# Kernel optimization log

Measured on AMD Instinct MI355X. Metric: run time of the kernel, lower is better.

## Reference

```python
import jax, jax.numpy as jnp
import numpy as np

N_NODES = 50000
N_EDGES = 800000
D_IN = 128
D_OUT = 128
ALPHA = 0.2  # LeakyReLU negative slope


def setup_inputs() -> dict:
    key = jax.random.key(0)
    k1, k2, k3, k4 = jax.random.split(key, 4)
    x = jax.random.normal(k1, (N_NODES, D_IN), dtype=jnp.float32)
    W = jax.random.normal(k2, (D_IN, D_OUT), dtype=jnp.float32) * (1.414 / np.sqrt(D_IN))
    a = jax.random.normal(k3, (2 * D_OUT, 1), dtype=jnp.float32) * 0.1
    edge_index = jax.random.randint(k4, (2, N_EDGES), 0, N_NODES, dtype=jnp.int64)
    return {"x": x, "W": W, "a": a, "edge_index": edge_index}


def reference(x, W, a, edge_index):
    # h: (N, D_OUT)
    h = x @ W
    src, dst = edge_index[0], edge_index[1]
    # e_i = leakyrelu([h[src]; h[dst]] @ a) == leakyrelu((h@a1)[src] + (h@a2)[dst])
    a1 = a[:D_OUT, 0]
    a2 = a[D_OUT:, 0]
    s1 = h @ a1  # (N,)
    s2 = h @ a2  # (N,)
    e = jax.nn.leaky_relu(s1[src] + s2[dst], negative_slope=ALPHA)  # (E,)
    # Global softmax over all edges (faithful to F.softmax(edge_e, dim=0))
    attention = jax.nn.softmax(e)  # (E,)
    # output[dst] += attention * h[src]  (scatter-add)
    msgs = attention[:, None] * h[src]  # (E, D_OUT)
    output = jax.ops.segment_sum(msgs, dst, num_segments=N_NODES)
    return output
```

## Files before the change

### kernel.cpp

```cpp
#include <hip/hip_runtime.h>
#include <hip/hip_bf16.h>

#define N_NODES 50000
#define N_EDGES 800000
#define D 128
#define ALPHA 0.2f
#define NEG_INF -1e30f

#define KB_BLOCKS 3125
#define NSCAN_BLOCKS ((N_NODES + 255) / 256)
#define LDS_STRIDE 272

typedef __attribute__((ext_vector_type(8))) short short8;
typedef __attribute__((ext_vector_type(4))) float floatx4;

__device__ __forceinline__ unsigned int f2bf(float v)
{
    __hip_bfloat16 b = __float2bfloat16(v);
    return (unsigned int)*reinterpret_cast<unsigned short*>(&b);
}
__device__ __forceinline__ float bf_lo(unsigned int u)
{
    return __uint_as_float(u << 16);
}
__device__ __forceinline__ float bf_hi(unsigned int u)
{
    return __uint_as_float(u & 0xFFFF0000u);
}

__global__ __launch_bounds__(256) void k_wprep(
    const float* __restrict__ W, const float* __restrict__ a,
    float* __restrict__ w12)
{
    const int t = threadIdx.x;
    const int i = t & 127;
    const int which = t >> 7;
    const float* av = a + which * D;
    float acc = 0.f;
    #pragma unroll 8
    for (int j = 0; j < D; ++j)
        acc += W[(size_t)i * D + j] * av[j];
    w12[which * D + i] = acc;
}

__global__ __launch_bounds__(256) void k_fused(
    const float* __restrict__ x, const float* __restrict__ W,
    const float* __restrict__ w12, const int* __restrict__ ei,
    unsigned short* __restrict__ hb, float* __restrict__ s1,
    float* __restrict__ s2, int* __restrict__ deg, int* __restrict__ rank)
{
    __shared__ unsigned char lds[16 * LDS_STRIDE];
    const int t = threadIdx.x;
    const int rowbase = blockIdx.x * 16;

    const int r = t >> 4;
    const int c = t & 15;
    const float* xp = x + (size_t)(rowbase + r) * D + c * 8;
    const float4 v0 = *(const float4*)(xp);
    const float4 v1 = *(const float4*)(xp + 4);

    const int lane = t & 63;
    const int wv = t >> 6;
    const int q = lane >> 4;
    const int nIdx = lane & 15;
    const int n0 = wv * 32;
    short8 B[2][4];
    #pragma unroll
    for (int kt = 0; kt < 4; ++kt) {
        short8 be, bo;
        #pragma unroll
        for (int j = 0; j < 8; ++j) {
            const float* wp = W + (size_t)(kt * 32 + q * 8 + j) * D + n0 + 2 * nIdx;
            be[j] = (short)f2bf(wp[0]);
            bo[j] = (short)f2bf(wp[1]);
        }
        B[0][kt] = be;
        B[1][kt] = bo;
    }

    {
        const float* w1 = w12 + c * 8;
        const float* w2 = w12 + D + c * 8;
        float p1 = v0.x * w1[0] + v0.y * w1[1] + v0.z * w1[2] + v0.w * w1[3]
                 + v1.x * w1[4] + v1.y * w1[5] + v1.z * w1[6] + v1.w * w1[7];
        float p2 = v0.x * w2[0] + v0.y * w2[1] + v0.z * w2[2] + v0.w * w2[3]
                 + v1.x * w2[4] + v1.y * w2[5] + v1.z * w2[6] + v1.w * w2[7];
        #pragma unroll
        for (int mask = 8; mask >= 1; mask >>= 1) {
            p1 += __shfl_xor(p1, mask);
            p2 += __shfl_xor(p2, mask);
        }
        if (c == 0) { s1[rowbase + r] = p1; s2[rowbase + r] = p2; }

        uint4 pk;
        pk.x = f2bf(v0.x) | (f2bf(v0.y) << 16);
        pk.y = f2bf(v0.z) | (f2bf(v0.w) << 16);
        pk.z = f2bf(v1.x) | (f2bf(v1.y) << 16);
        pk.w = f2bf(v1.z) | (f2bf(v1.w) << 16);
        *(uint4*)(lds + r * LDS_STRIDE + c * 16) = pk;
    }
    __syncthreads();

    const unsigned char* ab = lds + nIdx * LDS_STRIDE + q * 16;
    const short8 A0 = *(const short8*)(ab);
    const short8 A1 = *(const short8*)(ab + 64);
    const short8 A2 = *(const short8*)(ab + 128);
    const short8 A3 = *(const short8*)(ab + 192);

    floatx4 acc0 = {0.f, 0.f, 0.f, 0.f};
    floatx4 acc1 = {0.f, 0.f, 0.f, 0.f};
    acc0 = __builtin_amdgcn_mfma_f32_16x16x32_bf16(A0, B[0][0], acc0, 0, 0, 0);
    acc1 = __builtin_amdgcn_mfma_f32_16x16x32_bf16(A0, B[1][0], acc1, 0, 0, 0);
    acc0 = __builtin_amdgcn_mfma_f32_16x16x32_bf16(A1, B[0][1], acc0, 0, 0, 0);
    acc1 = __builtin_amdgcn_mfma_f32_16x16x32_bf16(A1, B[1][1], acc1, 0, 0, 0);
    acc0 = __builtin_amdgcn_mfma_f32_16x16x32_bf16(A2, B[0][2], acc0, 0, 0, 0);
    acc1 = __builtin_amdgcn_mfma_f32_16x16x32_bf16(A2, B[1][2], acc1, 0, 0, 0);
    acc0 = __builtin_amdgcn_mfma_f32_16x16x32_bf16(A3, B[0][3], acc0, 0, 0, 0);
    acc1 = __builtin_amdgcn_mfma_f32_16x16x32_bf16(A3, B[1][3], acc1, 0, 0, 0);

    #pragma unroll
    for (int i = 0; i < 4; ++i) {
        const int row = rowbase + q * 4 + i;
        const unsigned int pk = f2bf(acc0[i]) | (f2bf(acc1[i]) << 16);
        *(unsigned int*)(hb + (size_t)row * D + n0 + 2 * nIdx) = pk;
    }

    const int e = blockIdx.x * 256 + t;
    rank[e] = atomicAdd(&deg[ei[N_EDGES + e]], 1);
}

__device__ __forceinline__ void online_combine(float& m, float& s,
                                               float om, float os)
{
    float nm = fmaxf(m, om);
    s = s * __expf(m - nm) + os * __expf(om - nm);
    m = nm;
}

__global__ __launch_bounds__(256) void k_scan_a(
    const int* __restrict__ deg, int* __restrict__ partials)
{
    const int i = blockIdx.x * 256 + threadIdx.x;
    int v = (i < N_NODES) ? deg[i] : 0;
    #pragma unroll
    for (int off = 32; off >= 1; off >>= 1) v += __shfl_down(v, off);
    __shared__ int ws[4];
    if ((threadIdx.x & 63) == 0) ws[threadIdx.x >> 6] = v;
    __syncthreads();
    if (threadIdx.x == 0)
        partials[blockIdx.x] = ws[0] + ws[1] + ws[2] + ws[3];
}

__global__ __launch_bounds__(256) void k_scan_b(
    const int* __restrict__ partials, int* __restrict__ partialOffs,
    int* __restrict__ offs)
{
    __shared__ int sc[256];
    const int t = threadIdx.x;
    int v = (t < NSCAN_BLOCKS) ? partials[t] : 0;
    sc[t] = v;
    __syncthreads();
    #pragma unroll
    for (int off = 1; off < 256; off <<= 1) {
        int u = (t >= off) ? sc[t - off] : 0;
        __syncthreads();
        sc[t] += u;
        __syncthreads();
    }
    if (t < NSCAN_BLOCKS) partialOffs[t] = sc[t] - v;
    if (t == 255) offs[N_NODES] = sc[255];
}

__global__ __launch_bounds__(256) void k_scan_c(
    const int* __restrict__ deg, const int* __restrict__ partialOffs,
    int* __restrict__ offs)
{
    __shared__ int sc[256];
    const int t = threadIdx.x;
    const int i = blockIdx.x * 256 + t;
    const int v = (i < N_NODES) ? deg[i] : 0;
    sc[t] = v;
    __syncthreads();
    #pragma unroll
    for (int off = 1; off < 256; off <<= 1) {
        int u = (t >= off) ? sc[t - off] : 0;
        __syncthreads();
        sc[t] += u;
        __syncthreads();
    }
    if (i < N_NODES)
        offs[i] = partialOffs[blockIdx.x] + sc[t] - v;
}

__global__ __launch_bounds__(256) void k_bucket(
    const int* __restrict__ ei, const float* __restrict__ s1,
    const float* __restrict__ s2, const int* __restrict__ offs,
    const int* __restrict__ rank, unsigned int* __restrict__ csr,
    float* __restrict__ bm, float* __restrict__ bs)
{
    const int e = blockIdx.x * 256 + threadIdx.x;
    const int sN = ei[e];
    const int dN = ei[N_EDGES + e];
    csr[offs[dN] + rank[e]] = (unsigned int)sN;

    float v = s1[sN] + s2[dN];
    v = v > 0.f ? v : ALPHA * v;

    float m = v, s = 1.f;
    #pragma unroll
    for (int off = 32; off >= 1; off >>= 1) {
        float om = __shfl_down(m, off);
        float os = __shfl_down(s, off);
        online_combine(m, s, om, os);
    }
    __shared__ float rm[4], rs[4];
    const int wid = threadIdx.x >> 6;
    if ((threadIdx.x & 63) == 0) { rm[wid] = m; rs[wid] = s; }
    __syncthreads();
    if (threadIdx.x == 0) {
        #pragma unroll
        for (int w = 1; w < 4; ++w) online_combine(m, s, rm[w], rs[w]);
        bm[blockIdx.x] = m;
        bs[blockIdx.x] = s;
    }
}

__global__ __launch_bounds__(256) void k_reduce_mz(
    const float* __restrict__ bm, const float* __restrict__ bs,
    float* __restrict__ MZ)
{
    float m = NEG_INF, s = 0.f;
    for (int i = threadIdx.x; i < KB_BLOCKS; i += 256)
        online_combine(m, s, bm[i], bs[i]);
    #pragma unroll
    for (int off = 32; off >= 1; off >>= 1) {
        float om = __shfl_down(m, off);
        float os = __shfl_down(s, off);
        online_combine(m, s, om, os);
    }
    __shared__ float rm[4], rs[4];
    const int wid = threadIdx.x >> 6;
    if ((threadIdx.x & 63) == 0) { rm[wid] = m; rs[wid] = s; }
    __syncthreads();
    if (threadIdx.x == 0) {
        #pragma unroll
        for (int w = 1; w < 4; ++w) online_combine(m, s, rm[w], rs[w]);
        MZ[0] = m;
        MZ[1] = s;
    }
}

__global__ __launch_bounds__(256) void k_gather(
    const unsigned int* __restrict__ csr, const int* __restrict__ offs,
    const float* __restrict__ s1, const float* __restrict__ s2,
    const unsigned short* __restrict__ hb, const float* __restrict__ MZ,
    float* __restrict__ out)
{
    const int node = (blockIdx.x * blockDim.x + threadIdx.x) >> 6;
    if (node >= N_NODES) return;
    const int lane = threadIdx.x & 63;
    const float M = MZ[0];
    const float invZ = 1.0f / MZ[1];
    const float s2n = s2[node];
    const int beg = offs[node];
    const int end = offs[node + 1];

    float a0 = 0.f, a1 = 0.f, b0 = 0.f, b1 = 0.f;
    float c0 = 0.f, c1 = 0.f, d0 = 0.f, d1 = 0.f;

    for (int cb = beg; cb < end; cb += 64) {
        const int n = min(64, end - cb);
        const int srcl = (cb + lane < end) ? (int)csr[cb + lane] : 0;
        float v = s1[srcl] + s2n;
        v = v > 0.f ? v : ALPHA * v;
        const float attl = __expf(v - M) * invZ;

        int j = 0;
        for (; j + 3 < n; j += 4) {
            const int i0 = __shfl(srcl, j);
            const int i1 = __shfl(srcl, j + 1);
            const int i2 = __shfl(srcl, j + 2);
            const int i3 = __shfl(srcl, j + 3);
            const float w0 = __shfl(attl, j);
            const float w1 = __shfl(attl, j + 1);
            const float w2 = __shfl(attl, j + 2);
            const float w3 = __shfl(attl, j + 3);
            const unsigned int u0 =
                *(const unsigned int*)(hb + (size_t)i0 * D + lane * 2);
            const unsigned int u1 =
                *(const unsigned int*)(hb + (size_t)i1 * D + lane * 2);
            const unsigned int u2 =
                *(const unsigned int*)(hb + (size_t)i2 * D + lane * 2);
            const unsigned int u3 =
                *(const unsigned int*)(hb + (size_t)i3 * D + lane * 2);
            a0 += w0 * bf_lo(u0); a1 += w0 * bf_hi(u0);
            b0 += w1 * bf_lo(u1); b1 += w1 * bf_hi(u1);
            c0 += w2 * bf_lo(u2); c1 += w2 * bf_hi(u2);
            d0 += w3 * bf_lo(u3); d1 += w3 * bf_hi(u3);
        }
        for (; j < n; ++j) {
            const int i0 = __shfl(srcl, j);
            const float w0 = __shfl(attl, j);
            const unsigned int u0 =
                *(const unsigned int*)(hb + (size_t)i0 * D + lane * 2);
            a0 += w0 * bf_lo(u0); a1 += w0 * bf_hi(u0);
        }
    }
    float2 r;
    r.x = (a0 + b0) + (c0 + d0);
    r.y = (a1 + b1) + (c1 + d1);
    *(float2*)(out + (size_t)node * D + lane * 2) = r;
}

extern "C" void kernel_launch(void* const* d_in, const int* in_sizes, int n_in,
                              void* d_out, int out_size, void* d_ws, size_t ws_size,
                              hipStream_t stream)
{
    const float* x = (const float*)d_in[0];
    const float* W = (const float*)d_in[1];
    const float* a = (const float*)d_in[2];
    const int* ei = (const int*)d_in[3];
    float* out = (float*)d_out;

    char* wsb = (char*)d_ws;
    unsigned int* csr = (unsigned int*)wsb;
    unsigned short* hb = (unsigned short*)(wsb + (size_t)N_EDGES * 4);
    int* rank     = (int*)((char*)hb + (size_t)N_NODES * D * 2);
    float* s1     = (float*)(rank + N_EDGES);
    float* s2     = s1 + N_NODES;
    int*   deg    = (int*)(s2 + N_NODES);
    int*   offs   = deg + N_NODES;
    int*   partials    = offs + N_NODES + 1;
    int*   partialOffs = partials + NSCAN_BLOCKS;
    float* w12    = (float*)(partialOffs + NSCAN_BLOCKS);
    float* bm     = w12 + 2 * D;
    float* bs     = bm + KB_BLOCKS;
    float* MZ     = bs + KB_BLOCKS;

    hipMemsetAsync(deg, 0, N_NODES * sizeof(int), stream);

    k_wprep<<<1, 256, 0, stream>>>(W, a, w12);
    k_fused<<<N_NODES / 16, 256, 0, stream>>>(x, W, w12, ei, hb, s1, s2,
                                              deg, rank);
    k_scan_a<<<NSCAN_BLOCKS, 256, 0, stream>>>(deg, partials);
    k_scan_b<<<1, 256, 0, stream>>>(partials, partialOffs, offs);
    k_scan_c<<<NSCAN_BLOCKS, 256, 0, stream>>>(deg, partialOffs, offs);
    k_bucket<<<KB_BLOCKS, 256, 0, stream>>>(ei, s1, s2, offs, rank, csr,
                                            bm, bs);
    k_reduce_mz<<<1, 256, 0, stream>>>(bm, bs, MZ);
    k_gather<<<(N_NODES * 64 + 255) / 256, 256, 0, stream>>>(
        csr, offs, s1, s2, hb, MZ, out);
}
```

Baseline: 186.8 us.

## Cut kernel launches via grid-synced scan, last-block softmax reduce, and wider gather unroll

Folds the degree memset into the weight-prep kernel, and merges the three-pass scan into one kernel that spins on a global counter until all 196 blocks publish their sums. The separate max/sum reduction kernel is replaced by a last-block-done pattern inside the bucket kernel. The gather loop is unrolled to 8 edges with more accumulators to keep more loads in flight. This removes several launches and the gaps between them, but relies on all scan blocks being co-resident so the spin-wait cannot deadlock.

```diff
diff --git a/kernel.cpp b/kernel.cpp
--- a/kernel.cpp
+++ b/kernel.cpp
@@ -28,19 +28,24 @@
     return __uint_as_float(u & 0xFFFF0000u);
 }
 
-__global__ __launch_bounds__(256) void k_wprep(
+__global__ __launch_bounds__(256) void k_prep(
     const float* __restrict__ W, const float* __restrict__ a,
-    float* __restrict__ w12)
-{
-    const int t = threadIdx.x;
-    const int i = t & 127;
-    const int which = t >> 7;
-    const float* av = a + which * D;
-    float acc = 0.f;
-    #pragma unroll 8
-    for (int j = 0; j < D; ++j)
-        acc += W[(size_t)i * D + j] * av[j];
-    w12[which * D + i] = acc;
+    float* __restrict__ w12, int* __restrict__ deg, int* __restrict__ syncv)
+{
+    const int i = blockIdx.x * 256 + threadIdx.x;
+    if (i < N_NODES) deg[i] = 0;
+    if (i < 4) syncv[i] = 0;
+    if (blockIdx.x == 0) {
+        const int t = threadIdx.x;
+        const int r = t & 127;
+        const int which = t >> 7;
+        const float* av = a + which * D;
+        float acc = 0.f;
+        #pragma unroll 8
+        for (int j = 0; j < D; ++j)
+            acc += W[(size_t)r * D + j] * av[j];
+        w12[which * D + r] = acc;
+    }
 }
 
 __global__ __launch_bounds__(256) void k_fused(
@@ -137,27 +142,15 @@
     m = nm;
 }
 
-__global__ __launch_bounds__(256) void k_scan_a(
-    const int* __restrict__ deg, int* __restrict__ partials)
-{
-    const int i = blockIdx.x * 256 + threadIdx.x;
-    int v = (i < N_NODES) ? deg[i] : 0;
-    #pragma unroll
-    for (int off = 32; off >= 1; off >>= 1) v += __shfl_down(v, off);
-    __shared__ int ws[4];
-    if ((threadIdx.x & 63) == 0) ws[threadIdx.x >> 6] = v;
-    __syncthreads();
-    if (threadIdx.x == 0)
-        partials[blockIdx.x] = ws[0] + ws[1] + ws[2] + ws[3];
-}
-
-__global__ __launch_bounds__(256) void k_scan_b(
-    const int* __restrict__ partials, int* __restrict__ partialOffs,
-    int* __restrict__ offs)
+__global__ __launch_bounds__(256) void k_scan(
+    const int* __restrict__ deg, int* __restrict__ offs,
+    int* __restrict__ agg, int* __restrict__ cnt)
 {
     __shared__ int sc[256];
     const int t = threadIdx.x;
-    int v = (t < NSCAN_BLOCKS) ? partials[t] : 0;
+    const int b = blockIdx.x;
+    const int i = b * 256 + t;
+    const int v = (i < N_NODES) ? deg[i] : 0;
     sc[t] = v;
     __syncthreads();
     #pragma unroll
@@ -167,19 +160,21 @@
         sc[t] += u;
         __syncthreads();
     }
-    if (t < NSCAN_BLOCKS) partialOffs[t] = sc[t] - v;
-    if (t == 255) offs[N_NODES] = sc[255];
-}
-
-__global__ __launch_bounds__(256) void k_scan_c(
-    const int* __restrict__ deg, const int* __restrict__ partialOffs,
-    int* __restrict__ offs)
-{
-    __shared__ int sc[256];
-    const int t = threadIdx.x;
-    const int i = blockIdx.x * 256 + t;
-    const int v = (i < N_NODES) ? deg[i] : 0;
-    sc[t] = v;
+    const int excl = sc[t] - v;
+    if (t == 0) {
+        __hip_atomic_store(&agg[b], sc[255], __ATOMIC_RELAXED,
+                           __HIP_MEMORY_SCOPE_AGENT);
+        __hip_atomic_fetch_add(cnt, 1, __ATOMIC_RELEASE,
+                               __HIP_MEMORY_SCOPE_AGENT);
+        while (__hip_atomic_load(cnt, __ATOMIC_ACQUIRE,
+                                 __HIP_MEMORY_SCOPE_AGENT) < NSCAN_BLOCKS) {}
+    }
+    __syncthreads();
+
+    int av = (t < NSCAN_BLOCKS)
+        ? __hip_atomic_load(&agg[t], __ATOMIC_RELAXED, __HIP_MEMORY_SCOPE_AGENT)
+        : 0;
+    sc[t] = av;
     __syncthreads();
     #pragma unroll
     for (int off = 1; off < 256; off <<= 1) {
@@ -188,15 +183,17 @@
         sc[t] += u;
         __syncthreads();
     }
-    if (i < N_NODES)
-        offs[i] = partialOffs[blockIdx.x] + sc[t] - v;
+    const int prefix = (b == 0) ? 0 : sc[b - 1];
+    if (i < N_NODES) offs[i] = prefix + excl;
+    if (b == 0 && t == 0) offs[N_NODES] = N_EDGES;
 }
 
 __global__ __launch_bounds__(256) void k_bucket(
     const int* __restrict__ ei, const float* __restrict__ s1,
     const float* __restrict__ s2, const int* __restrict__ offs,
     const int* __restrict__ rank, unsigned int* __restrict__ csr,
-    float* __restrict__ bm, float* __restrict__ bs)
+    float* __restrict__ bm, float* __restrict__ bs, int* __restrict__ cnt,
+    float* __restrict__ MZ)
 {
     const int e = blockIdx.x * 256 + threadIdx.x;
     const int sN = ei[e];
@@ -214,39 +211,45 @@
         online_combine(m, s, om, os);
     }
     __shared__ float rm[4], rs[4];
+    __shared__ int lastFlag;
     const int wid = threadIdx.x >> 6;
     if ((threadIdx.x & 63) == 0) { rm[wid] = m; rs[wid] = s; }
     __syncthreads();
     if (threadIdx.x == 0) {
         #pragma unroll
         for (int w = 1; w < 4; ++w) online_combine(m, s, rm[w], rs[w]);
-        bm[blockIdx.x] = m;
-        bs[blockIdx.x] = s;
-    }
-}
-
-__global__ __launch_bounds__(256) void k_reduce_mz(
-    const float* __restrict__ bm, const float* __restrict__ bs,
-    float* __restrict__ MZ)
-{
-    float m = NEG_INF, s = 0.f;
-    for (int i = threadIdx.x; i < KB_BLOCKS; i += 256)
-        online_combine(m, s, bm[i], bs[i]);
+        __hip_atomic_store(&bm[blockIdx.x], m, __ATOMIC_RELAXED,
+                           __HIP_MEMORY_SCOPE_AGENT);
+        __hip_atomic_store(&bs[blockIdx.x], s, __ATOMIC_RELAXED,
+                           __HIP_MEMORY_SCOPE_AGENT);
+        const int done = __hip_atomic_fetch_add(cnt, 1, __ATOMIC_ACQ_REL,
+                                                __HIP_MEMORY_SCOPE_AGENT);
+        lastFlag = (done == KB_BLOCKS - 1);
+    }
+    __syncthreads();
+    if (!lastFlag) return;
+
+    float mm = NEG_INF, ss = 0.f;
+    for (int j = threadIdx.x; j < KB_BLOCKS; j += 256) {
+        const float om = __hip_atomic_load(&bm[j], __ATOMIC_RELAXED,
+                                           __HIP_MEMORY_SCOPE_AGENT);
+        const float os = __hip_atomic_load(&bs[j], __ATOMIC_RELAXED,
+                                           __HIP_MEMORY_SCOPE_AGENT);
+        online_combine(mm, ss, om, os);
+    }
     #pragma unroll
     for (int off = 32; off >= 1; off >>= 1) {
-        float om = __shfl_down(m, off);
-        float os = __shfl_down(s, off);
-        online_combine(m, s, om, os);
-    }
-    __shared__ float rm[4], rs[4];
-    const int wid = threadIdx.x >> 6;
-    if ((threadIdx.x & 63) == 0) { rm[wid] = m; rs[wid] = s; }
+        float om = __shfl_down(mm, off);
+        float os = __shfl_down(ss, off);
+        online_combine(mm, ss, om, os);
+    }
+    if ((threadIdx.x & 63) == 0) { rm[wid] = mm; rs[wid] = ss; }
     __syncthreads();
     if (threadIdx.x == 0) {
         #pragma unroll
-        for (int w = 1; w < 4; ++w) online_combine(m, s, rm[w], rs[w]);
-        MZ[0] = m;
-        MZ[1] = s;
+        for (int w = 1; w < 4; ++w) online_combine(mm, ss, rm[w], rs[w]);
+        MZ[0] = mm;
+        MZ[1] = ss;
     }
 }
 
@@ -267,6 +270,8 @@
 
     float a0 = 0.f, a1 = 0.f, b0 = 0.f, b1 = 0.f;
     float c0 = 0.f, c1 = 0.f, d0 = 0.f, d1 = 0.f;
+    float e0 = 0.f, e1 = 0.f, f0 = 0.f, f1 = 0.f;
+    float g0 = 0.f, g1 = 0.f, h0 = 0.f, h1 = 0.f;
 
     for (int cb = beg; cb < end; cb += 64) {
         const int n = min(64, end - cb);
@@ -276,6 +281,40 @@
         const float attl = __expf(v - M) * invZ;
 
         int j = 0;
+        for (; j + 7 < n; j += 8) {
+            const int i0 = __shfl(srcl, j);
+            const int i1 = __shfl(srcl, j + 1);
+            const int i2 = __shfl(srcl, j + 2);
+            const int i3 = __shfl(srcl, j + 3);
+            const int i4 = __shfl(srcl, j + 4);
+            const int i5 = __shfl(srcl, j + 5);
+            const int i6 = __shfl(srcl, j + 6);
+            const int i7 = __shfl(srcl, j + 7);
+            const float w0 = __shfl(attl, j);
+            const float w1 = __shfl(attl, j + 1);
+            const float w2 = __shfl(attl, j + 2);
+            const float w3 = __shfl(attl, j + 3);
+            const float w4 = __shfl(attl, j + 4);
+            const float w5 = __shfl(attl, j + 5);
+            const float w6 = __shfl(attl, j + 6);
+            const float w7 = __shfl(attl, j + 7);
+            const unsigned int u0 = *(const unsigned int*)(hb + (size_t)i0 * D + lane * 2);
+            const unsigned int u1 = *(const unsigned int*)(hb + (size_t)i1 * D + lane * 2);
+            const unsigned int u2 = *(const unsigned int*)(hb + (size_t)i2 * D + lane * 2);
+            const unsigned int u3 = *(const unsigned int*)(hb + (size_t)i3 * D + lane * 2);
+            const unsigned int u4 = *(const unsigned int*)(hb + (size_t)i4 * D + lane * 2);
+            const unsigned int u5 = *(const unsigned int*)(hb + (size_t)i5 * D + lane * 2);
+            const unsigned int u6 = *(const unsigned int*)(hb + (size_t)i6 * D + lane * 2);
+            const unsigned int u7 = *(const unsigned int*)(hb + (size_t)i7 * D + lane * 2);
+            a0 += w0 * bf_lo(u0); a1 += w0 * bf_hi(u0);
+            b0 += w1 * bf_lo(u1); b1 += w1 * bf_hi(u1);
+            c0 += w2 * bf_lo(u2); c1 += w2 * bf_hi(u2);
+            d0 += w3 * bf_lo(u3); d1 += w3 * bf_hi(u3);
+            e0 += w4 * bf_lo(u4); e1 += w4 * bf_hi(u4);
+            f0 += w5 * bf_lo(u5); f1 += w5 * bf_hi(u5);
+            g0 += w6 * bf_lo(u6); g1 += w6 * bf_hi(u6);
+            h0 += w7 * bf_lo(u7); h1 += w7 * bf_hi(u7);
+        }
         for (; j + 3 < n; j += 4) {
             const int i0 = __shfl(srcl, j);
             const int i1 = __shfl(srcl, j + 1);
@@ -285,14 +324,10 @@
             const float w1 = __shfl(attl, j + 1);
             const float w2 = __shfl(attl, j + 2);
             const float w3 = __shfl(attl, j + 3);
-            const unsigned int u0 =
-                *(const unsigned int*)(hb + (size_t)i0 * D + lane * 2);
-            const unsigned int u1 =
-                *(const unsigned int*)(hb + (size_t)i1 * D + lane * 2);
-            const unsigned int u2 =
-                *(const unsigned int*)(hb + (size_t)i2 * D + lane * 2);
-            const unsigned int u3 =
-                *(const unsigned int*)(hb + (size_t)i3 * D + lane * 2);
+            const unsigned int u0 = *(const unsigned int*)(hb + (size_t)i0 * D + lane * 2);
+            const unsigned int u1 = *(const unsigned int*)(hb + (size_t)i1 * D + lane * 2);
+            const unsigned int u2 = *(const unsigned int*)(hb + (size_t)i2 * D + lane * 2);
+            const unsigned int u3 = *(const unsigned int*)(hb + (size_t)i3 * D + lane * 2);
             a0 += w0 * bf_lo(u0); a1 += w0 * bf_hi(u0);
             b0 += w1 * bf_lo(u1); b1 += w1 * bf_hi(u1);
             c0 += w2 * bf_lo(u2); c1 += w2 * bf_hi(u2);
@@ -301,14 +336,13 @@
         for (; j < n; ++j) {
             const int i0 = __shfl(srcl, j);
             const float w0 = __shfl(attl, j);
-            const unsigned int u0 =
-                *(const unsigned int*)(hb + (size_t)i0 * D + lane * 2);
+            const unsigned int u0 = *(const unsigned int*)(hb + (size_t)i0 * D + lane * 2);
             a0 += w0 * bf_lo(u0); a1 += w0 * bf_hi(u0);
         }
     }
     float2 r;
-    r.x = (a0 + b0) + (c0 + d0);
-    r.y = (a1 + b1) + (c1 + d1);
+    r.x = ((a0 + b0) + (c0 + d0)) + ((e0 + f0) + (g0 + h0));
+    r.y = ((a1 + b1) + (c1 + d1)) + ((e1 + f1) + (g1 + h1));
     *(float2*)(out + (size_t)node * D + lane * 2) = r;
 }
 
@@ -330,24 +364,19 @@
     float* s2     = s1 + N_NODES;
     int*   deg    = (int*)(s2 + N_NODES);
     int*   offs   = deg + N_NODES;
-    int*   partials    = offs + N_NODES + 1;
-    int*   partialOffs = partials + NSCAN_BLOCKS;
-    float* w12    = (float*)(partialOffs + NSCAN_BLOCKS);
+    int*   agg    = offs + N_NODES + 1;
+    int*   syncv  = agg + NSCAN_BLOCKS;
+    float* w12    = (float*)(syncv + 4);
     float* bm     = w12 + 2 * D;
     float* bs     = bm + KB_BLOCKS;
     float* MZ     = bs + KB_BLOCKS;
 
-    hipMemsetAsync(deg, 0, N_NODES * sizeof(int), stream);
-
-    k_wprep<<<1, 256, 0, stream>>>(W, a, w12);
+    k_prep<<<NSCAN_BLOCKS, 256, 0, stream>>>(W, a, w12, deg, syncv);
     k_fused<<<N_NODES / 16, 256, 0, stream>>>(x, W, w12, ei, hb, s1, s2,
                                               deg, rank);
-    k_scan_a<<<NSCAN_BLOCKS, 256, 0, stream>>>(deg, partials);
-    k_scan_b<<<1, 256, 0, stream>>>(partials, partialOffs, offs);
-    k_scan_c<<<NSCAN_BLOCKS, 256, 0, stream>>>(deg, partialOffs, offs);
+    k_scan<<<NSCAN_BLOCKS, 256, 0, stream>>>(deg, offs, agg, syncv + 0);
     k_bucket<<<KB_BLOCKS, 256, 0, stream>>>(ei, s1, s2, offs, rank, csr,
-                                            bm, bs);
-    k_reduce_mz<<<1, 256, 0, stream>>>(bm, bs, MZ);
+                                            bm, bs, syncv + 1, MZ);
     k_gather<<<(N_NODES * 64 + 255) / 256, 256, 0, stream>>>(
         csr, offs, s1, s2, hb, MZ, out);
 }
```

Result: slower. 299.7 us (+60.4%).
